# Kernel tuning notes

Hardware: AMD Instinct MI355X
Metric: run time of the kernel (lower is better)

## Reference

```python
import jax, jax.numpy as jnp
import numpy as np

V, E, H, L, S, B = 32000, 1024, 512, 2, 512, 32  # vocab, emb dim, per-dir hidden, layers, seq, batch
PAD = 0
assert E == 2 * H  # required by the module's pred_emb shape assert; lets cell weights stack


def setup_inputs() -> dict:
    ks = iter(jax.random.split(jax.random.key(0), 40))
    def nrm(shape, scale=0.05):
        return jax.random.normal(next(ks), shape, dtype=jnp.float32) * scale
    seq_input = jax.random.randint(next(ks), (S, B), 1, V)
    # lengths sorted descending (pack_padded convention the torch code assumes)
    lengths = jnp.sort(jax.random.randint(next(ks), (B,), S // 2, S + 1))[::-1]
    inp = {"seq_input": seq_input, "lengths": lengths}
    for name in ("emb1", "emb2", "emb3"):
        inp[name] = nrm((V, E)).at[PAD].set(0.0)  # padding_idx row is zero
    inp["W_et"] = nrm((H, E)); inp["b_et"] = nrm((H,))      # embedding_transform
    inp["W_ct"] = nrm((H, H)); inp["b_ct"] = nrm((H,))      # context_transform
    inp["W_sc"] = nrm((1, H)); inp["b_sc"] = nrm((1,))      # to_scalar
    inp["W_g"] = nrm((E, 2 * E)); inp["b_g"] = nrm((E,))    # embedding_gate Linear
    inp["h0f"] = jax.random.uniform(next(ks), (H,), jnp.float32)  # torch.rand init params
    inp["c0f"] = jax.random.uniform(next(ks), (H,), jnp.float32)
    inp["h0b"] = jax.random.uniform(next(ks), (H,), jnp.float32)
    inp["c0b"] = jax.random.uniform(next(ks), (H,), jnp.float32)
    # LSTMCell weights: [layer, dir(fwd,bwd), 4H, in]; in==E==2H for all layers
    inp["Wih"] = nrm((L, 2, 4 * H, E))
    inp["Whh"] = nrm((L, 2, 4 * H, H))
    inp["bih"] = nrm((L, 2, 4 * H))
    inp["bhh"] = nrm((L, 2, 4 * H))
    return inp


def _lstm_cell(x, h, c, Wih, Whh, bih, bhh):
    g = x @ Wih.T + h @ Whh.T + bih + bhh
    i, f, gg, o = jnp.split(g, 4, axis=-1)
    c2 = jax.nn.sigmoid(f) * c + jax.nn.sigmoid(i) * jnp.tanh(gg)
    return jax.nn.sigmoid(o) * jnp.tanh(c2), c2


def _reverse_seq(x, lengths):
    # reverse the first `length` timesteps per batch element, keep padding in place
    t = jnp.arange(x.shape[0])[:, None]
    idx = jnp.where(t < lengths[None, :], lengths[None, :] - 1 - t, t)  # [S,B]
    idx = idx.reshape(idx.shape + (1,) * (x.ndim - 2))
    return jnp.take_along_axis(x, jnp.broadcast_to(idx, x.shape), axis=0)


def _cos(a, b):
    n = jnp.sum(a * b, -1)
    d = jnp.maximum(jnp.linalg.norm(a, axis=-1) * jnp.linalg.norm(b, axis=-1), 1e-8)
    return n / d


def _forward(seq_input, lengths, emb1, emb2, emb3, W_et, b_et, W_ct, b_ct, W_sc, b_sc,
             W_g, b_g, h0f, c0f, h0b, c0b, Wih, Whh, bih, bhh):
    Sl, Bn = seq_input.shape
    Hh = Whh.shape[-1]
    nL = Wih.shape[0]
    # active mask at step t: lengths >= t+1 (identical for forward and reversed scans)
    mask = jnp.arange(Sl)[:, None] < lengths[None, :]  # [S,B]
    h0f_b = jnp.broadcast_to(h0f, (Bn, Hh)); c0f_b = jnp.broadcast_to(c0f, (Bn, Hh))
    h0b_b = jnp.broadcast_to(h0b, (Bn, Hh)); c0b_b = jnp.broadcast_to(c0b, (Bn, Hh))
    cell = lambda l, d: (Wih[l, d], Whh[l, d], bih[l, d], bhh[l, d])

    def layer0_scan(tokens, cell_p, h0, c0):
        def step(carry, inp):
            h, c, pen = carry
            tok, m = inp
            e1, e2, e3 = emb1[tok], emb2[tok], emb3[tok]  # [B,E]
            p = (jax.nn.relu(_cos(e1, e2) - 0.3) + jax.nn.relu(_cos(e1, e3) - 0.3)
                 + jax.nn.relu(_cos(e2, e3) - 0.3))
            pen = pen + jnp.sum(jnp.where(m, p, 0.0))
            ctx = h @ W_ct.T + b_ct  # [B,H]
            sc = lambda e: jnp.tanh(e @ W_et.T + b_et + ctx) @ W_sc.T + b_sc  # [B,1]
            w = jax.nn.softmax(jnp.concatenate([sc(e1), sc(e2), sc(e3)], -1), axis=-1)
            x = w[:, :1] * e1 + w[:, 1:2] * e2 + w[:, 2:3] * e3  # attended embedding
            h2, c2 = _lstm_cell(x, h, c, *cell_p)
            mm = m[:, None]
            h = jnp.where(mm, h2, h)
            c = jnp.where(mm, c2, c)
            return (h, c, pen), (jnp.where(mm, h2, 0.0), jnp.where(mm, x, 0.0))
        (hf, cf, pen), (outs, preds) = jax.lax.scan(
            step, (h0, c0, jnp.zeros((), jnp.float32)), (tokens, mask))
        return hf, cf, outs, pen, preds

    def layer_scan(xs, cell_p, h0, c0):
        def step(carry, inp):
            h, c = carry
            x, m = inp
            h2, c2 = _lstm_cell(x, h, c, *cell_p)
            mm = m[:, None]
            return (jnp.where(mm, h2, h), jnp.where(mm, c2, c)), jnp.where(mm, h2, 0.0)
        (hf, cf), outs = jax.lax.scan(step, (h0, c0), (xs, mask))
        return hf, cf, outs

    # layer 0 with embedding attention + cosine penalty
    hF, cF, outF, penF, predF = layer0_scan(seq_input, cell(0, 0), h0f_b, c0f_b)
    hB, cB, outB, penB, predB = layer0_scan(_reverse_seq(seq_input, lengths), cell(0, 1), h0b_b, c0b_b)
    penalty = penF + penB
    predB = _reverse_seq(predB, lengths)
    gate = jax.nn.sigmoid(jnp.concatenate([predF, predB], -1) @ W_g.T + b_g)
    pred_emb = predF * gate + predB * (1.0 - gate)
    x = jnp.concatenate([outF, _reverse_seq(outB, lengths)], -1)  # [S,B,2H]
    hs = [hF, hB]; cs = [cF, cB]
    for l in range(1, nL):
        hF, cF, oF = layer_scan(x, cell(l, 0), h0f_b, c0f_b)
        hB, cB, oB = layer_scan(_reverse_seq(x, lengths), cell(l, 1), h0b_b, c0b_b)
        x = jnp.concatenate([oF, _reverse_seq(oB, lengths)], -1)
        hs += [hF, hB]; cs += [cF, cB]
    final_h = jnp.stack(hs, 0)  # [2L,B,H]
    final_c = jnp.stack(cs, 0)
    return final_h, final_c, x, penalty, pred_emb


def reference(seq_input, lengths, emb1, emb2, emb3, W_et, b_et, W_ct, b_ct, W_sc, b_sc,
              W_g, b_g, h0f, c0f, h0b, c0b, Wih, Whh, bih, bhh):
    return _forward(seq_input, lengths, emb1, emb2, emb3, W_et, b_et, W_ct, b_ct, W_sc,
                    b_sc, W_g, b_g, h0f, c0f, h0b, c0b, Wih, Whh, bih, bhh)
```

## Files before the change

### kernel.cpp

```cpp
#include <hip/hip_runtime.h>

typedef unsigned short u16;
typedef unsigned long long u64;
typedef __bf16 bf16_t;
typedef bf16_t bf16x8 __attribute__((ext_vector_type(8)));
typedef float f32x4 __attribute__((ext_vector_type(4)));

#define DEVFN static __device__ __forceinline__

constexpr int S_ = 512, B_ = 32, H_ = 512, E_ = 1024;
constexpr int SB_ = S_ * B_;

constexpr size_t OUT_FH  = 0;
constexpr size_t OUT_FC  = 65536;
constexpr size_t OUT_X   = 131072;
constexpr size_t OUT_PEN = 16908288;
constexpr size_t OUT_PE  = 16908289;

constexpr size_t WS_SLOTS = 0;
constexpr size_t WS_STAG  = 4096;
constexpr size_t WS_PEN   = 6144;
constexpr size_t WS_SPART = 6400;
constexpr size_t WS_HG    = 30976;
constexpr size_t WS_WET   = 237824;
constexpr size_t WS_WCT   = 1286400;
constexpr size_t WS_WIH0  = 1810688;
constexpr size_t WS_WHH0  = 10199296;
constexpr size_t WS_WIH1  = 14393600;
constexpr size_t WS_WHH1  = 22782208;
constexpr size_t WS_WG    = 26976512;
constexpr size_t WS_EK    = 31170816;
constexpr size_t WS_ET    = 131834112;
constexpr size_t WS_PREDF = 232497408;
constexpr size_t WS_PREDB = 266051840;
constexpr size_t WS_OUT0F = 299606272;
constexpr size_t WS_OUT0B = 316383488;

DEVFN u16 f2bf(float f) {
  union { float f; unsigned u; } v; v.f = f;
  unsigned u = v.u;
  unsigned r = (u + 0x7fffu + ((u >> 16) & 1u)) >> 16;
  return (u16)r;
}
DEVFN float bf2f(u16 h) {
  union { unsigned u; float f; } v; v.u = ((unsigned)h) << 16;
  return v.f;
}
DEVFN float sigm(float x) { return 1.f / (1.f + __expf(-x)); }
DEVFN float tanh_f(float x) { float e = __expf(2.f * x); return 1.f - 2.f / (e + 1.f); }
DEVFN bf16x8 ld_bf8(const u16* p) { return *reinterpret_cast<const bf16x8*>(p); }
DEVFN f32x4 mfma_bf(bf16x8 a, bf16x8 b, f32x4 c) {
  return __builtin_amdgcn_mfma_f32_16x16x32_bf16(a, b, c, 0, 0, 0);
}
DEVFN void lds_st16(u16* base, int row, int rowBytes, int byteCol, bf16x8 v) {
  *reinterpret_cast<bf16x8*>((char*)base + row * rowBytes + (byteCol ^ ((row & 7) << 4))) = v;
}
DEVFN bf16x8 lds_ld16(const u16* base, int row, int rowBytes, int byteCol) {
  return *reinterpret_cast<const bf16x8*>((const char*)base + row * rowBytes + (byteCol ^ ((row & 7) << 4)));
}

DEVFN u64 coh_ld64(const u64* p) {
  return __hip_atomic_load(p, __ATOMIC_RELAXED, __HIP_MEMORY_SCOPE_AGENT);
}
DEVFN void coh_st64(u64* p, u64 v) {
  __hip_atomic_store(p, v, __ATOMIC_RELAXED, __HIP_MEMORY_SCOPE_AGENT);
}
DEVFN unsigned coh_ld32(const unsigned* p) {
  return __hip_atomic_load(p, __ATOMIC_RELAXED, __HIP_MEMORY_SCOPE_AGENT);
}
DEVFN void coh_st32(unsigned* p, unsigned v) {
  __hip_atomic_store(p, v, __ATOMIC_RELAXED, __HIP_MEMORY_SCOPE_AGENT);
}
DEVFN void wave_vmcnt0() { asm volatile("s_waitcnt vmcnt(0)" ::: "memory"); }

DEVFN void poll64(const unsigned* tags, unsigned target) {
  int lane = threadIdx.x & 63;
  for (;;) {
    unsigned v = coh_ld32(tags + lane * 4);
    if (__all(v >= target)) break;
    __builtin_amdgcn_s_sleep(1);
  }
  asm volatile("" ::: "memory");
}

__global__ void k_f2bf(const float* __restrict__ src, u16* __restrict__ dst, int n) {
  for (int i = blockIdx.x * blockDim.x + threadIdx.x; i < n; i += gridDim.x * blockDim.x)
    dst[i] = f2bf(src[i]);
}

__global__ __launch_bounds__(256) void k_gather(
    const int* __restrict__ seq, const int* __restrict__ lengths,
    const float* __restrict__ emb1, const float* __restrict__ emb2, const float* __restrict__ emb3,
    u16* __restrict__ eK, float* __restrict__ pen) {
  int s = blockIdx.x;
  int t = s >> 5, b = s & 31;
  int tid = threadIdx.x;
  int tok = seq[s];
  const float4* p1 = (const float4*)(emb1 + (size_t)tok * 1024);
  const float4* p2 = (const float4*)(emb2 + (size_t)tok * 1024);
  const float4* p3 = (const float4*)(emb3 + (size_t)tok * 1024);
  float4 a = p1[tid], c = p2[tid], d = p3[tid];
  size_t rb = (size_t)s * 1024 + tid * 4;
  uint2 pk;
  pk.x = f2bf(a.x) | ((unsigned)f2bf(a.y) << 16); pk.y = f2bf(a.z) | ((unsigned)f2bf(a.w) << 16);
  *(uint2*)(eK + rb) = pk;
  pk.x = f2bf(c.x) | ((unsigned)f2bf(c.y) << 16); pk.y = f2bf(c.z) | ((unsigned)f2bf(c.w) << 16);
  *(uint2*)(eK + (size_t)SB_ * 1024 + rb) = pk;
  pk.x = f2bf(d.x) | ((unsigned)f2bf(d.y) << 16); pk.y = f2bf(d.z) | ((unsigned)f2bf(d.w) << 16);
  *(uint2*)(eK + (size_t)2 * SB_ * 1024 + rb) = pk;
  float v[6];
  v[0] = a.x*c.x + a.y*c.y + a.z*c.z + a.w*c.w;
  v[1] = a.x*d.x + a.y*d.y + a.z*d.z + a.w*d.w;
  v[2] = c.x*d.x + c.y*d.y + c.z*d.z + c.w*d.w;
  v[3] = a.x*a.x + a.y*a.y + a.z*a.z + a.w*a.w;
  v[4] = c.x*c.x + c.y*c.y + c.z*c.z + c.w*c.w;
  v[5] = d.x*d.x + d.y*d.y + d.z*d.z + d.w*d.w;
  for (int i = 0; i < 6; ++i)
    for (int m = 1; m < 64; m <<= 1) v[i] += __shfl_xor(v[i], m);
  __shared__ float red[4][6];
  int wid = tid >> 6, lane = tid & 63;
  if (lane == 0) for (int i = 0; i < 6; ++i) red[wid][i] = v[i];
  __syncthreads();
  if (tid == 0) {
    float r[6];
    for (int i = 0; i < 6; ++i) r[i] = red[0][i] + red[1][i] + red[2][i] + red[3][i];
    float c12 = r[0] / fmaxf(sqrtf(r[3]) * sqrtf(r[4]), 1e-8f);
    float c13 = r[1] / fmaxf(sqrtf(r[3]) * sqrtf(r[5]), 1e-8f);
    float c23 = r[2] / fmaxf(sqrtf(r[4]) * sqrtf(r[5]), 1e-8f);
    float p = fmaxf(c12 - 0.3f, 0.f) + fmaxf(c13 - 0.3f, 0.f) + fmaxf(c23 - 0.3f, 0.f);
    if (t < lengths[b] && p > 0.f) atomicAdd(pen, 2.f * p);
  }
}

__global__ __launch_bounds__(256) void k_gemm_et(
    const u16* __restrict__ A, const u16* __restrict__ Bw,
    const float* __restrict__ bias, float* __restrict__ C) {
  int bm = blockIdx.x % 384, bn = blockIdx.x / 384;
  int m0 = bm * 128, n0 = bn * 128;
  __shared__ u16 sA[128 * 64], sB[128 * 64];
  int tid = threadIdx.x, wid = tid >> 6, lane = tid & 63;
  int wm = wid & 1, wn = wid >> 1;
  f32x4 acc[4][4] = {};
  for (int kb = 0; kb < 16; ++kb) {
    __syncthreads();
    for (int c = tid; c < 1024; c += 256) {
      int row = c >> 3, q = c & 7;
      lds_st16(sA, row, 128, q * 16, ld_bf8(A + (size_t)(m0 + row) * 1024 + kb * 64 + q * 8));
      lds_st16(sB, row, 128, q * 16, ld_bf8(Bw + (size_t)(n0 + row) * 1024 + kb * 64 + q * 8));
    }
    __syncthreads();
    for (int kk = 0; kk < 2; ++kk) {
      bf16x8 af[4], bf[4];
      int bc = kk * 64 + (lane >> 4) * 16;
      for (int i = 0; i < 4; ++i) {
        af[i] = lds_ld16(sA, wm * 64 + i * 16 + (lane & 15), 128, bc);
        bf[i] = lds_ld16(sB, wn * 64 + i * 16 + (lane & 15), 128, bc);
      }
      for (int i = 0; i < 4; ++i)
        for (int j = 0; j < 4; ++j) acc[i][j] = mfma_bf(af[i], bf[j], acc[i][j]);
    }
  }
  for (int i = 0; i < 4; ++i)
    for (int j = 0; j < 4; ++j) {
      int m = m0 + wm * 64 + i * 16 + (lane >> 4) * 4;
      int n = n0 + wn * 64 + j * 16 + (lane & 15);
      float bn_ = bias[n & 511];
      for (int r = 0; r < 4; ++r) C[(size_t)(m + r) * 512 + n] = acc[i][j][r] + bn_;
    }
}

__global__ __launch_bounds__(256) void k_gemm_gate(
    const u16* __restrict__ pF, const u16* __restrict__ pB, const u16* __restrict__ Wg,
    const float* __restrict__ bias, float* __restrict__ outPE) {
  int bm = blockIdx.x % 128, bn = blockIdx.x / 128;
  int m0 = bm * 128, n0 = bn * 128;
  __shared__ u16 sA[128 * 64], sB[128 * 64];
  int tid = threadIdx.x, wid = tid >> 6, lane = tid & 63;
  int wm = wid & 1, wn = wid >> 1;
  f32x4 acc[4][4] = {};
  for (int kb = 0; kb < 32; ++kb) {
    __syncthreads();
    const u16* Asrc = (kb < 16) ? pF : pB;
    int kof = (kb < 16) ? kb * 64 : (kb - 16) * 64;
    for (int c = tid; c < 1024; c += 256) {
      int row = c >> 3, q = c & 7;
      lds_st16(sA, row, 128, q * 16, ld_bf8(Asrc + (size_t)(m0 + row) * 1024 + kof + q * 8));
      lds_st16(sB, row, 128, q * 16, ld_bf8(Wg + (size_t)(n0 + row) * 2048 + kb * 64 + q * 8));
    }
    __syncthreads();
    for (int kk = 0; kk < 2; ++kk) {
      bf16x8 af[4], bf[4];
      int bc = kk * 64 + (lane >> 4) * 16;
      for (int i = 0; i < 4; ++i) {
        af[i] = lds_ld16(sA, wm * 64 + i * 16 + (lane & 15), 128, bc);
        bf[i] = lds_ld16(sB, wn * 64 + i * 16 + (lane & 15), 128, bc);
      }
      for (int i = 0; i < 4; ++i)
        for (int j = 0; j < 4; ++j) acc[i][j] = mfma_bf(af[i], bf[j], acc[i][j]);
    }
  }
  for (int i = 0; i < 4; ++i)
    for (int j = 0; j < 4; ++j) {
      int m = m0 + wm * 64 + i * 16 + (lane >> 4) * 4;
      int n = n0 + wn * 64 + j * 16 + (lane & 15);
      float bn_ = bias[n];
      for (int r = 0; r < 4; ++r) {
        float g = sigm(acc[i][j][r] + bn_);
        size_t idx = (size_t)(m + r) * 1024 + n;
        float a = bf2f(pF[idx]), b = bf2f(pB[idx]);
        outPE[idx] = a * g + b * (1.f - g);
      }
    }
}

__global__ __launch_bounds__(256, 1) void k_scan0(
    const u16* __restrict__ eK, const float* __restrict__ eT,
    const u16* __restrict__ wIh0, const u16* __restrict__ wHh0, const u16* __restrict__ wCt,
    const float* __restrict__ Wsc, const float* __restrict__ bct,
    const float* __restrict__ bih, const float* __restrict__ bhh,
    const int* __restrict__ lengths,
    const float* __restrict__ h0f, const float* __restrict__ c0f,
    const float* __restrict__ h0b, const float* __restrict__ c0b,
    u16* __restrict__ hg, float* __restrict__ spart,
    u16* __restrict__ out0F, u16* __restrict__ out0B,
    u16* __restrict__ predF, u16* __restrict__ predB,
    float* __restrict__ dout, unsigned* __restrict__ slots, unsigned* __restrict__ stag) {
  const int dir = blockIdx.x >> 6;
  const int r   = blockIdx.x & 63;
  const int tid = threadIdx.x, wid = tid >> 6, lane = tid & 63;

  const u16* Wih = wIh0 + (size_t)dir * 2048 * 1024;
  const u16* Whh = wHh0 + (size_t)dir * 2048 * 512;
  const float* bi = bih + dir * 2048;
  const float* bh = bhh + dir * 2048;
  u16* out0 = dir ? out0B : out0F;
  u16* predD = dir ? predB : predF;
  const float* h0 = dir ? h0b : h0f;
  const float* c0 = dir ? c0b : c0f;
  u16* myhg = hg + (size_t)dir * 2 * 32 * 512;
  float* spartD = spart + (size_t)dir * 3 * 32 * 32;
  unsigned* slotg = slots + dir * 64 * 4;
  unsigned* stagD = stag + dir * 64 * 4;

  __shared__ u16 sWih[32 * 1024];
  __shared__ u16 sWhh[32 * 512];
  __shared__ u16 sHpub[256];
  __shared__ float sPW[3][32][32];
  __shared__ float sHW[32][32];
  __shared__ float sSK[3][32];
  __shared__ float sWt[32][4];
  __shared__ float sBias[32];

  for (int c = tid; c < 4096; c += 256) {
    int ln = c >> 7, q = c & 127;
    int n = (ln >> 3) * 512 + r * 8 + (ln & 7);
    lds_st16(sWih, ln, 2048, q * 16, ld_bf8(Wih + (size_t)n * 1024 + q * 8));
  }
  for (int c = tid; c < 2048; c += 256) {
    int ln = c >> 6, q = c & 63;
    int n = (ln >> 3) * 512 + r * 8 + (ln & 7);
    lds_st16(sWhh, ln, 1024, q * 16, ld_bf8(Whh + (size_t)n * 512 + q * 8));
  }
  if (tid < 32) {
    int n = (tid >> 3) * 512 + r * 8 + (tid & 7);
    sBias[tid] = bi[n] + bh[n];
  }

  const int pb = tid >> 3, pj = tid & 7;
  const int gj = r * 8 + pj;
  float hreg = h0[gj], creg = c0[gj];
  const int lenb = lengths[pb];
  const int Lmax = lengths[0];

  const int Mt = wid & 1, Nt = wid >> 1;
  const int arow = Mt * 16 + (lane & 15);
  const int lenrow = lengths[arow];
  const int kq = lane >> 4;
  const int colN = Nt * 16 + (lane & 15);
  const bool isctx = (r < 32) && (wid < 2);
  int lctx[4];
  if (isctx)
    for (int reg = 0; reg < 4; ++reg) lctx[reg] = lengths[Mt * 16 + kq * 4 + reg];

  sHpub[tid] = f2bf(hreg);
  __syncthreads();
  if (wid == 0) {
    u64 v = *reinterpret_cast<const u64*>(sHpub + lane * 4);
    coh_st64((u64*)myhg + (size_t)(lane >> 1) * 128 + r * 2 + (lane & 1), v);
    wave_vmcnt0();
    if (lane == 0) coh_st32(slotg + r * 4, 1u);
  }
  if (wid == 0) poll64(slotg, 1u);
  __syncthreads();

  float petU[3][4];
  if (isctx) {
    int j = r * 16 + (lane & 15);
    for (int reg = 0; reg < 4; ++reg) {
      int b = Mt * 16 + kq * 4 + reg;
      int lb = lctx[reg];
      int pos = (dir == 0) ? 0 : (lb - 1);
      size_t rowoff = (size_t)(pos * 32 + b) * 512 + j;
      for (int k = 0; k < 3; ++k) petU[k][reg] = eT[(size_t)k * SB_ * 512 + rowoff];
    }
  }

  for (int t = 0; t < Lmax; ++t) {
    const bool last = (t == Lmax - 1);
    bf16x8 hf[16];
    {
      const u64* hrow = (const u64*)(myhg + (size_t)(t & 1) * 32 * 512) +
                        (size_t)arow * 128 + kq * 2;
      u64 lo[16], hi[16];
#pragma unroll
      for (int kb = 0; kb < 16; ++kb) {
        lo[kb] = coh_ld64(hrow + kb * 8);
        hi[kb] = coh_ld64(hrow + kb * 8 + 1);
      }
#pragma unroll
      for (int kb = 0; kb < 16; ++kb) {
        union { u64 q[2]; bf16x8 v; } u; u.q[0] = lo[kb]; u.q[1] = hi[kb];
        hf[kb] = u.v;
      }
    }
    {
      f32x4 acc = {0.f, 0.f, 0.f, 0.f};
#pragma unroll
      for (int kb = 0; kb < 16; ++kb)
        acc = mfma_bf(hf[kb], lds_ld16(sWhh, colN, 1024, (kb * 32 + kq * 8) * 2), acc);
      int rb = Mt * 16 + kq * 4;
      for (int reg = 0; reg < 4; ++reg) sHW[rb + reg][colN] = acc[reg];
    }
    if (isctx) {
      f32x4 acc = {0.f, 0.f, 0.f, 0.f};
      int j = r * 16 + (lane & 15);
      const u16* Wctp = wCt + (size_t)j * 512;
#pragma unroll
      for (int kb = 0; kb < 16; ++kb)
        acc = mfma_bf(hf[kb], ld_bf8(Wctp + kb * 32 + kq * 8), acc);
      float wsc = Wsc[j], bctj = bct[j];
      for (int k = 0; k < 3; ++k)
        for (int reg = 0; reg < 4; ++reg) {
          float v = tanh_f(petU[k][reg] + acc[reg] + bctj) * wsc;
          v += __shfl_xor(v, 1); v += __shfl_xor(v, 2);
          v += __shfl_xor(v, 4); v += __shfl_xor(v, 8);
          if ((lane & 15) == 0) {
            int b = Mt * 16 + kq * 4 + reg;
            union { float f; unsigned u; } w; w.f = v;
            coh_st32((unsigned*)(spartD + (k * 32 + b) * 32 + r), w.u);
          }
        }
      wave_vmcnt0();
      if (lane == 0) coh_st32(stagD + (r * 2 + Mt) * 4, (unsigned)(t + 1));
    }
    float petN[3][4];
    if (isctx && t + 1 < Lmax) {
      int j = r * 16 + (lane & 15);
      for (int reg = 0; reg < 4; ++reg) {
        int b = Mt * 16 + kq * 4 + reg;
        int lb = lctx[reg];
        int tn = t + 1;
        int pos = (dir == 0) ? tn : ((tn < lb) ? (lb - 1 - tn) : tn);
        size_t rowoff = (size_t)(pos * 32 + b) * 512 + j;
        for (int k = 0; k < 3; ++k) petN[k][reg] = eT[(size_t)k * SB_ * 512 + rowoff];
      }
    }
    {
      int posA = (dir == 0) ? t : ((t < lenrow) ? (lenrow - 1 - t) : t);
      size_t ebase = (size_t)(posA * 32 + arow) * 1024;
      for (int k = 0; k < 3; ++k) {
        const u16* Ek = eK + (size_t)k * SB_ * 1024 + ebase;
        f32x4 acc = {0.f, 0.f, 0.f, 0.f};
#pragma unroll 4
        for (int kb = 0; kb < 32; ++kb)
          acc = mfma_bf(ld_bf8(Ek + kb * 32 + kq * 8),
                        lds_ld16(sWih, colN, 2048, (kb * 32 + kq * 8) * 2), acc);
        int rb = Mt * 16 + kq * 4;
        for (int reg = 0; reg < 4; ++reg) sPW[k][rb + reg][colN] = acc[reg];
      }
    }
    if (wid < 2) poll64(stagD, (unsigned)(t + 1));
    if (tid < 96) {
      int k = tid >> 5, b = tid & 31;
      const u64* sp = (const u64*)(spartD + (k * 32 + b) * 32);
      float s = 0.f;
#pragma unroll
      for (int i = 0; i < 16; ++i) {
        union { u64 u; float f[2]; } w; w.u = coh_ld64(sp + i);
        s += w.f[0] + w.f[1];
      }
      sSK[k][b] = s;
    }
    __syncthreads();
    if (tid < 32) {
      float s0 = sSK[0][tid], s1 = sSK[1][tid], s2 = sSK[2][tid];
      float mx = fmaxf(s0, fmaxf(s1, s2));
      float e0 = __expf(s0 - mx), e1 = __expf(s1 - mx), e2 = __expf(s2 - mx);
      float inv = 1.f / (e0 + e1 + e2);
      sWt[tid][0] = e0 * inv; sWt[tid][1] = e1 * inv; sWt[tid][2] = e2 * inv;
    }
    __syncthreads();
    float w0 = sWt[pb][0], w1 = sWt[pb][1], w2 = sWt[pb][2];
    float h2, c2; bool m; int pos;
    {
      float gq[4];
      for (int q = 0; q < 4; ++q) {
        int cl = q * 8 + pj;
        gq[q] = w0 * sPW[0][pb][cl] + w1 * sPW[1][pb][cl] + w2 * sPW[2][pb][cl]
              + sHW[pb][cl] + sBias[cl];
      }
      float ig = sigm(gq[0]), fg = sigm(gq[1]), gg = tanh_f(gq[2]), og = sigm(gq[3]);
      c2 = fg * creg + ig * gg;
      h2 = og * tanh_f(c2);
      m = (t < lenb);
      if (m) { creg = c2; hreg = h2; }
      pos = (dir == 0) ? t : ((t < lenb) ? (lenb - 1 - t) : t);
      sHpub[tid] = f2bf(hreg);
    }
    __syncthreads();
    if (!last && wid == 0) {
      u64 v = *reinterpret_cast<const u64*>(sHpub + lane * 4);
      coh_st64((u64*)(myhg + (size_t)((t + 1) & 1) * 32 * 512) +
               (size_t)(lane >> 1) * 128 + r * 2 + (lane & 1), v);
      wave_vmcnt0();
      if (lane == 0) coh_st32(slotg + r * 4, (unsigned)(t + 2));
    }
    {
      out0[(size_t)(pos * 32 + pb) * 512 + gj] = f2bf(m ? h2 : 0.f);
      size_t rowb = (size_t)(pos * 32 + pb) * 1024;
      int e0i = r * 16 + (tid & 7) * 2;
      for (int ii = 0; ii < 2; ++ii) {
        int e = e0i + ii;
        float xv = w0 * bf2f(eK[rowb + e])
                 + w1 * bf2f(eK[(size_t)SB_ * 1024 + rowb + e])
                 + w2 * bf2f(eK[(size_t)2 * SB_ * 1024 + rowb + e]);
        predD[rowb + e] = f2bf(m ? xv : 0.f);
      }
    }
    if (isctx)
      for (int k = 0; k < 3; ++k)
        for (int reg = 0; reg < 4; ++reg) petU[k][reg] = petN[k][reg];
    if (!last) {
      if (wid == 0) poll64(slotg, (unsigned)(t + 2));
      __syncthreads();
    }
  }

  dout[OUT_FH + ((size_t)dir * 32 + pb) * 512 + gj] = hreg;
  dout[OUT_FC + ((size_t)dir * 32 + pb) * 512 + gj] = creg;
  for (int row = Lmax * 32 + r; row < SB_; row += 64) {
    if (tid < 128) ((u64*)(out0 + (size_t)row * 512))[tid] = 0;
    ((u64*)(predD + (size_t)row * 1024))[tid] = 0;
  }
}

__global__ __launch_bounds__(256, 1) void k_scan1(
    const u16* __restrict__ out0F, const u16* __restrict__ out0B,
    const u16* __restrict__ wIh1, const u16* __restrict__ wHh1,
    const float* __restrict__ bih, const float* __restrict__ bhh,
    const int* __restrict__ lengths,
    const float* __restrict__ h0f, const float* __restrict__ c0f,
    const float* __restrict__ h0b, const float* __restrict__ c0b,
    u16* __restrict__ hg, float* __restrict__ dout, unsigned* __restrict__ slots) {
  const int dir = blockIdx.x >> 6;
  const int r   = blockIdx.x & 63;
  const int tid = threadIdx.x, wid = tid >> 6, lane = tid & 63;

  const u16* Wih = wIh1 + (size_t)dir * 2048 * 1024;
  const u16* Whh = wHh1 + (size_t)dir * 2048 * 512;
  const float* bi = bih + (2 + dir) * 2048;
  const float* bh = bhh + (2 + dir) * 2048;
  const float* h0 = dir ? h0b : h0f;
  const float* c0 = dir ? c0b : c0f;
  unsigned* slotg = slots + (2 + dir) * 64 * 4;

  __shared__ u16 sWih[32 * 1024];
  __shared__ u16 sWhh[32 * 512];
  __shared__ u16 sHpub[256];
  __shared__ float sG[32][32];
  __shared__ float sBias[32];

  for (int c = tid; c < 4096; c += 256) {
    int ln = c >> 7, q = c & 127;
    int n = (ln >> 3) * 512 + r * 8 + (ln & 7);
    lds_st16(sWih, ln, 2048, q * 16, ld_bf8(Wih + (size_t)n * 1024 + q * 8));
  }
  for (int c = tid; c < 2048; c += 256) {
    int ln = c >> 6, q = c & 63;
    int n = (ln >> 3) * 512 + r * 8 + (ln & 7);
    lds_st16(sWhh, ln, 1024, q * 16, ld_bf8(Whh + (size_t)n * 512 + q * 8));
  }
  if (tid < 32) {
    int n = (tid >> 3) * 512 + r * 8 + (tid & 7);
    sBias[tid] = bi[n] + bh[n];
  }

  const int pb = tid >> 3, pj = tid & 7;
  const int gj = r * 8 + pj;
  float hreg = h0[gj], creg = c0[gj];
  const int lenb = lengths[pb];
  const int Lmax = lengths[0];
  const int Mt = wid & 1, Nt = wid >> 1;
  const int arow = Mt * 16 + (lane & 15);
  const int lenrow = lengths[arow];
  const int kq = lane >> 4;
  const int colN = Nt * 16 + (lane & 15);

  __syncthreads();
  f32x4 accx = {0.f, 0.f, 0.f, 0.f};
  {
    int posA = (dir == 0) ? 0 : (lenrow - 1);
    size_t rowb = (size_t)(posA * 32 + arow) * 512;
#pragma unroll 4
    for (int kb = 0; kb < 32; ++kb) {
      const u16* Asrc = (kb < 16) ? (out0F + rowb + kb * 32 + kq * 8)
                                  : (out0B + rowb + (kb - 16) * 32 + kq * 8);
      accx = mfma_bf(ld_bf8(Asrc), lds_ld16(sWih, colN, 2048, (kb * 32 + kq * 8) * 2), accx);
    }
  }

  sHpub[tid] = f2bf(hreg);
  __syncthreads();
  if (wid == 0) {
    u64 v = *reinterpret_cast<const u64*>(sHpub + lane * 4);
    coh_st64((u64*)(hg + (size_t)(0 * 2 + dir) * 32 * 512) +
             (size_t)(lane >> 1) * 128 + r * 2 + (lane & 1), v);
    wave_vmcnt0();
    if (lane == 0) coh_st32(slotg + r * 4, 1u);
  }
  if (wid == 0) poll64(slotg, 1u);
  __syncthreads();

  for (int t = 0; t < Lmax; ++t) {
    const bool last = (t == Lmax - 1);
    bf16x8 hf[16];
    {
      const u64* hrow = (const u64*)(hg + (size_t)((t & 1) * 2 + dir) * 32 * 512) +
                        (size_t)arow * 128 + kq * 2;
      u64 lo[16], hi[16];
#pragma unroll
      for (int kb = 0; kb < 16; ++kb) {
        lo[kb] = coh_ld64(hrow + kb * 8);
        hi[kb] = coh_ld64(hrow + kb * 8 + 1);
      }
#pragma unroll
      for (int kb = 0; kb < 16; ++kb) {
        union { u64 q[2]; bf16x8 v; } u; u.q[0] = lo[kb]; u.q[1] = hi[kb];
        hf[kb] = u.v;
      }
    }
    f32x4 acc = accx;
#pragma unroll
    for (int kb = 0; kb < 16; ++kb)
      acc = mfma_bf(hf[kb], lds_ld16(sWhh, colN, 1024, (kb * 32 + kq * 8) * 2), acc);
    {
      int rb = Mt * 16 + kq * 4;
      for (int reg = 0; reg < 4; ++reg) sG[rb + reg][colN] = acc[reg];
    }
    __syncthreads();
    float h2, c2; bool m; int pos;
    {
      float gq[4];
      for (int q = 0; q < 4; ++q) gq[q] = sG[pb][q * 8 + pj] + sBias[q * 8 + pj];
      float ig = sigm(gq[0]), fg = sigm(gq[1]), gg = tanh_f(gq[2]), og = sigm(gq[3]);
      c2 = fg * creg + ig * gg;
      h2 = og * tanh_f(c2);
      m = (t < lenb);
      if (m) { creg = c2; hreg = h2; }
      pos = (dir == 0) ? t : ((t < lenb) ? (lenb - 1 - t) : t);
      sHpub[tid] = f2bf(hreg);
    }
    __syncthreads();
    if (!last && wid == 0) {
      u64 v = *reinterpret_cast<const u64*>(sHpub + lane * 4);
      coh_st64((u64*)(hg + (size_t)(((t + 1) & 1) * 2 + dir) * 32 * 512) +
               (size_t)(lane >> 1) * 128 + r * 2 + (lane & 1), v);
      wave_vmcnt0();
      if (lane == 0) coh_st32(slotg + r * 4, (unsigned)(t + 2));
    }
    dout[OUT_X + (size_t)(pos * 32 + pb) * 1024 + dir * 512 + gj] = m ? h2 : 0.f;
    if (!last) {
      int tn = t + 1;
      int posA = (dir == 0) ? tn : ((tn < lenrow) ? (lenrow - 1 - tn) : tn);
      size_t rowb = (size_t)(posA * 32 + arow) * 512;
      f32x4 ax = {0.f, 0.f, 0.f, 0.f};
#pragma unroll 4
      for (int kb = 0; kb < 32; ++kb) {
        const u16* Asrc = (kb < 16) ? (out0F + rowb + kb * 32 + kq * 8)
                                    : (out0B + rowb + (kb - 16) * 32 + kq * 8);
        ax = mfma_bf(ld_bf8(Asrc), lds_ld16(sWih, colN, 2048, (kb * 32 + kq * 8) * 2), ax);
      }
      accx = ax;
      if (wid == 0) poll64(slotg, (unsigned)(t + 2));
      __syncthreads();
    }
  }

  dout[OUT_FH + ((size_t)(2 + dir) * 32 + pb) * 512 + gj] = hreg;
  dout[OUT_FC + ((size_t)(2 + dir) * 32 + pb) * 512 + gj] = creg;
  for (int row = Lmax * 32 + r; row < SB_; row += 64) {
    ((u64*)(dout + OUT_X + (size_t)row * 1024 + dir * 512))[tid] = 0;
  }
}

__global__ void k_final(const float* __restrict__ pen, float* __restrict__ dout) {
  if (threadIdx.x == 0 && blockIdx.x == 0) dout[OUT_PEN] = pen[0];
}

extern "C" void kernel_launch(void* const* d_in, const int* in_sizes, int n_in,
                              void* d_out, int out_size, void* d_ws, size_t ws_size,
                              hipStream_t stream) {
  (void)in_sizes; (void)n_in; (void)out_size; (void)ws_size;
  const int*   seq   = (const int*)d_in[0];
  const int*   lens  = (const int*)d_in[1];
  const float* emb1  = (const float*)d_in[2];
  const float* emb2  = (const float*)d_in[3];
  const float* emb3  = (const float*)d_in[4];
  const float* W_et  = (const float*)d_in[5];
  const float* b_et  = (const float*)d_in[6];
  const float* W_ct  = (const float*)d_in[7];
  const float* b_ct  = (const float*)d_in[8];
  const float* W_sc  = (const float*)d_in[9];
  const float* W_g   = (const float*)d_in[11];
  const float* b_g   = (const float*)d_in[12];
  const float* h0f   = (const float*)d_in[13];
  const float* c0f   = (const float*)d_in[14];
  const float* h0b   = (const float*)d_in[15];
  const float* c0b   = (const float*)d_in[16];
  const float* Wih   = (const float*)d_in[17];
  const float* Whh   = (const float*)d_in[18];
  const float* bih   = (const float*)d_in[19];
  const float* bhh   = (const float*)d_in[20];
  float* out = (float*)d_out;
  char* ws = (char*)d_ws;

  unsigned* slots = (unsigned*)(ws + WS_SLOTS);
  unsigned* stag  = (unsigned*)(ws + WS_STAG);
  float* pen    = (float*)(ws + WS_PEN);
  float* spart  = (float*)(ws + WS_SPART);
  u16* hgbuf = (u16*)(ws + WS_HG);
  u16* wEt  = (u16*)(ws + WS_WET);
  u16* wCt  = (u16*)(ws + WS_WCT);
  u16* wIh0 = (u16*)(ws + WS_WIH0);
  u16* wHh0 = (u16*)(ws + WS_WHH0);
  u16* wIh1 = (u16*)(ws + WS_WIH1);
  u16* wHh1 = (u16*)(ws + WS_WHH1);
  u16* wGg  = (u16*)(ws + WS_WG);
  u16* eK   = (u16*)(ws + WS_EK);
  float* eT = (float*)(ws + WS_ET);
  u16* pF   = (u16*)(ws + WS_PREDF);
  u16* pB   = (u16*)(ws + WS_PREDB);
  u16* o0F  = (u16*)(ws + WS_OUT0F);
  u16* o0B  = (u16*)(ws + WS_OUT0B);

  hipMemsetAsync(ws, 0, 6400, stream);

  hipLaunchKernelGGL(k_f2bf, dim3(512), dim3(256), 0, stream, W_et, wEt, 524288);
  hipLaunchKernelGGL(k_f2bf, dim3(512), dim3(256), 0, stream, W_ct, wCt, 262144);
  hipLaunchKernelGGL(k_f2bf, dim3(2048), dim3(256), 0, stream, Wih, wIh0, 4194304);
  hipLaunchKernelGGL(k_f2bf, dim3(2048), dim3(256), 0, stream, Wih + 4194304, wIh1, 4194304);
  hipLaunchKernelGGL(k_f2bf, dim3(1024), dim3(256), 0, stream, Whh, wHh0, 2097152);
  hipLaunchKernelGGL(k_f2bf, dim3(1024), dim3(256), 0, stream, Whh + 2097152, wHh1, 2097152);
  hipLaunchKernelGGL(k_f2bf, dim3(1024), dim3(256), 0, stream, W_g, wGg, 2097152);

  hipLaunchKernelGGL(k_gather, dim3(SB_), dim3(256), 0, stream,
                     seq, lens, emb1, emb2, emb3, eK, pen);
  hipLaunchKernelGGL(k_gemm_et, dim3(1536), dim3(256), 0, stream, eK, wEt, b_et, eT);
  hipLaunchKernelGGL(k_scan0, dim3(128), dim3(256), 0, stream,
                     eK, eT, wIh0, wHh0, wCt, W_sc, b_ct, bih, bhh, lens,
                     h0f, c0f, h0b, c0b, hgbuf, spart, o0F, o0B, pF, pB, out, slots, stag);
  hipLaunchKernelGGL(k_scan1, dim3(128), dim3(256), 0, stream,
                     o0F, o0B, wIh1, wHh1, bih, bhh, lens,
                     h0f, c0f, h0b, c0b, hgbuf, out, slots);
  hipLaunchKernelGGL(k_gemm_gate, dim3(1024), dim3(256), 0, stream,
                     pF, pB, wGg, b_g, out + OUT_PE);
  hipLaunchKernelGGL(k_final, dim3(1), dim3(64), 0, stream, pen, out);
}
```

Before: 16.69 ms.

## Stage hidden state through LDS with coalesced loads and overlap with embedding MFMA

Each step's published hidden state is now read from global memory with coalesced 64-bit loads spread over all threads and staged into a swizzled LDS buffer. Waves then read their MFMA A-fragments from LDS instead of each issuing its own strided coherent global loads. In layer 0, the first embedding-projection GEMM is moved between issuing those loads and storing them to LDS, so the global latency can overlap with compute. This adds a block barrier and 32KB of LDS per kernel, which may lower occupancy or lengthen the per-step critical path.

```diff
diff --git a/kernel.cpp b/kernel.cpp
--- a/kernel.cpp
+++ b/kernel.cpp
@@ -54,6 +54,9 @@
 }
 DEVFN void lds_st16(u16* base, int row, int rowBytes, int byteCol, bf16x8 v) {
   *reinterpret_cast<bf16x8*>((char*)base + row * rowBytes + (byteCol ^ ((row & 7) << 4))) = v;
+}
+DEVFN void lds_st8(u16* base, int row, int rowBytes, int byteCol, u64 v) {
+  *reinterpret_cast<u64*>((char*)base + row * rowBytes + (byteCol ^ ((row & 7) << 4))) = v;
 }
 DEVFN bf16x8 lds_ld16(const u16* base, int row, int rowBytes, int byteCol) {
   return *reinterpret_cast<const bf16x8*>((const char*)base + row * rowBytes + (byteCol ^ ((row & 7) << 4)));
@@ -244,6 +247,7 @@
 
   __shared__ u16 sWih[32 * 1024];
   __shared__ u16 sWhh[32 * 512];
+  __shared__ u16 sH[32 * 512];
   __shared__ u16 sHpub[256];
   __shared__ float sPW[3][32][32];
   __shared__ float sHW[32][32];
@@ -307,27 +311,36 @@
 
   for (int t = 0; t < Lmax; ++t) {
     const bool last = (t == Lmax - 1);
-    bf16x8 hf[16];
-    {
-      const u64* hrow = (const u64*)(myhg + (size_t)(t & 1) * 32 * 512) +
-                        (size_t)arow * 128 + kq * 2;
-      u64 lo[16], hi[16];
-#pragma unroll
-      for (int kb = 0; kb < 16; ++kb) {
-        lo[kb] = coh_ld64(hrow + kb * 8);
-        hi[kb] = coh_ld64(hrow + kb * 8 + 1);
-      }
-#pragma unroll
-      for (int kb = 0; kb < 16; ++kb) {
-        union { u64 q[2]; bf16x8 v; } u; u.q[0] = lo[kb]; u.q[1] = hi[kb];
-        hf[kb] = u.v;
-      }
-    }
-    {
+    int posA = (dir == 0) ? t : ((t < lenrow) ? (lenrow - 1 - t) : t);
+    size_t ebase = (size_t)(posA * 32 + arow) * 1024;
+    u64 hv[16];
+    {
+      const u64* src = (const u64*)(myhg + (size_t)(t & 1) * 32 * 512);
+#pragma unroll
+      for (int i = 0; i < 16; ++i) hv[i] = coh_ld64(src + tid + i * 256);
+    }
+    {
+      const u16* Ek = eK + ebase;
       f32x4 acc = {0.f, 0.f, 0.f, 0.f};
+#pragma unroll 4
+      for (int kb = 0; kb < 32; ++kb)
+        acc = mfma_bf(ld_bf8(Ek + kb * 32 + kq * 8),
+                      lds_ld16(sWih, colN, 2048, (kb * 32 + kq * 8) * 2), acc);
+      int rb = Mt * 16 + kq * 4;
+      for (int reg = 0; reg < 4; ++reg) sPW[0][rb + reg][colN] = acc[reg];
+    }
+#pragma unroll
+    for (int i = 0; i < 16; ++i) {
+      int c = tid + i * 256, row = c >> 7, q = c & 127;
+      lds_st8(sH, row, 1024, q * 8, hv[i]);
+    }
+    __syncthreads();
+    {
+      f32x4 acc = {0.f, 0.f, 0.f, 0.f};
 #pragma unroll
       for (int kb = 0; kb < 16; ++kb)
-        acc = mfma_bf(hf[kb], lds_ld16(sWhh, colN, 1024, (kb * 32 + kq * 8) * 2), acc);
+        acc = mfma_bf(lds_ld16(sH, arow, 1024, (kb * 32 + kq * 8) * 2),
+                      lds_ld16(sWhh, colN, 1024, (kb * 32 + kq * 8) * 2), acc);
       int rb = Mt * 16 + kq * 4;
       for (int reg = 0; reg < 4; ++reg) sHW[rb + reg][colN] = acc[reg];
     }
@@ -337,7 +350,8 @@
       const u16* Wctp = wCt + (size_t)j * 512;
 #pragma unroll
       for (int kb = 0; kb < 16; ++kb)
-        acc = mfma_bf(hf[kb], ld_bf8(Wctp + kb * 32 + kq * 8), acc);
+        acc = mfma_bf(lds_ld16(sH, arow, 1024, (kb * 32 + kq * 8) * 2),
+                      ld_bf8(Wctp + kb * 32 + kq * 8), acc);
       float wsc = Wsc[j], bctj = bct[j];
       for (int k = 0; k < 3; ++k)
         for (int reg = 0; reg < 4; ++reg) {
@@ -365,19 +379,15 @@
         for (int k = 0; k < 3; ++k) petN[k][reg] = eT[(size_t)k * SB_ * 512 + rowoff];
       }
     }
-    {
-      int posA = (dir == 0) ? t : ((t < lenrow) ? (lenrow - 1 - t) : t);
-      size_t ebase = (size_t)(posA * 32 + arow) * 1024;
-      for (int k = 0; k < 3; ++k) {
-        const u16* Ek = eK + (size_t)k * SB_ * 1024 + ebase;
-        f32x4 acc = {0.f, 0.f, 0.f, 0.f};
+    for (int k = 1; k < 3; ++k) {
+      const u16* Ek = eK + (size_t)k * SB_ * 1024 + ebase;
+      f32x4 acc = {0.f, 0.f, 0.f, 0.f};
 #pragma unroll 4
-        for (int kb = 0; kb < 32; ++kb)
-          acc = mfma_bf(ld_bf8(Ek + kb * 32 + kq * 8),
-                        lds_ld16(sWih, colN, 2048, (kb * 32 + kq * 8) * 2), acc);
-        int rb = Mt * 16 + kq * 4;
-        for (int reg = 0; reg < 4; ++reg) sPW[k][rb + reg][colN] = acc[reg];
-      }
+      for (int kb = 0; kb < 32; ++kb)
+        acc = mfma_bf(ld_bf8(Ek + kb * 32 + kq * 8),
+                      lds_ld16(sWih, colN, 2048, (kb * 32 + kq * 8) * 2), acc);
+      int rb = Mt * 16 + kq * 4;
+      for (int reg = 0; reg < 4; ++reg) sPW[k][rb + reg][colN] = acc[reg];
     }
     if (wid < 2) poll64(stagD, (unsigned)(t + 1));
     if (tid < 96) {
@@ -476,6 +486,7 @@
 
   __shared__ u16 sWih[32 * 1024];
   __shared__ u16 sWhh[32 * 512];
+  __shared__ u16 sH[32 * 512];
   __shared__ u16 sHpub[256];
   __shared__ float sG[32][32];
   __shared__ float sBias[32];
@@ -533,26 +544,23 @@
 
   for (int t = 0; t < Lmax; ++t) {
     const bool last = (t == Lmax - 1);
-    bf16x8 hf[16];
-    {
-      const u64* hrow = (const u64*)(hg + (size_t)((t & 1) * 2 + dir) * 32 * 512) +
-                        (size_t)arow * 128 + kq * 2;
-      u64 lo[16], hi[16];
-#pragma unroll
-      for (int kb = 0; kb < 16; ++kb) {
-        lo[kb] = coh_ld64(hrow + kb * 8);
-        hi[kb] = coh_ld64(hrow + kb * 8 + 1);
-      }
-#pragma unroll
-      for (int kb = 0; kb < 16; ++kb) {
-        union { u64 q[2]; bf16x8 v; } u; u.q[0] = lo[kb]; u.q[1] = hi[kb];
-        hf[kb] = u.v;
-      }
-    }
+    {
+      const u64* src = (const u64*)(hg + (size_t)((t & 1) * 2 + dir) * 32 * 512);
+      u64 hv[16];
+#pragma unroll
+      for (int i = 0; i < 16; ++i) hv[i] = coh_ld64(src + tid + i * 256);
+#pragma unroll
+      for (int i = 0; i < 16; ++i) {
+        int c = tid + i * 256, row = c >> 7, q = c & 127;
+        lds_st8(sH, row, 1024, q * 8, hv[i]);
+      }
+    }
+    __syncthreads();
     f32x4 acc = accx;
 #pragma unroll
     for (int kb = 0; kb < 16; ++kb)
-      acc = mfma_bf(hf[kb], lds_ld16(sWhh, colN, 1024, (kb * 32 + kq * 8) * 2), acc);
+      acc = mfma_bf(lds_ld16(sH, arow, 1024, (kb * 32 + kq * 8) * 2),
+                    lds_ld16(sWhh, colN, 1024, (kb * 32 + kq * 8) * 2), acc);
     {
       int rb = Mt * 16 + kq * 4;
       for (int reg = 0; reg < 4; ++reg) sG[rb + reg][colN] = acc[reg];
```

Result: faster. 14.34 ms, median of 2 (-14.1%).
